# Optimization experiments

Hardware: AMD Instinct MI355X
Metric: run time of the kernel (lower is better)

Reference implementation:

```python
import jax, jax.numpy as jnp
import numpy as np

L, N, D_IN = 4, 2048, 1024
H, DH = 8, 64
INNER = H * DH          # 512
D_OUT = D_IN            # out_dim defaults to input_dim
SCALE = DH ** -0.5


def setup_inputs() -> dict:
    key = jax.random.key(0)
    ks = jax.random.split(key, 7)
    x = jax.random.normal(ks[0], (L, N, D_IN), jnp.float32)
    # torch Linear weights are [out_features, in_features]; xavier-ish scale
    Wq = jax.random.normal(ks[1], (INNER, D_IN), jnp.float32) * 0.03
    Wk = jax.random.normal(ks[2], (INNER, D_IN), jnp.float32) * 0.03
    Wv = jax.random.normal(ks[3], (INNER, D_IN), jnp.float32) * 0.03
    Wo = jax.random.normal(ks[4], (D_OUT, INNER), jnp.float32) * 0.03
    bo = jnp.zeros((D_OUT,), jnp.float32)
    # boolean key-padding mask [L, n]; ensure at least one valid key per row
    mask = jax.random.uniform(ks[5], (L, N)) < 0.9
    mask = mask.at[:, 0].set(True)
    return {"x": x, "Wq": Wq, "Wk": Wk, "Wv": Wv, "Wo": Wo, "bo": bo, "mask": mask}


def reference(x, Wq, Wk, Wv, Wo, bo, mask):
    # projections (Linear: y = x @ W^T), split heads: L n (h d) -> l h n d
    def split_heads(t):
        return t.reshape(L, N, H, DH).transpose(0, 2, 1, 3)

    q = split_heads(jnp.einsum('lnd,ed->lne', x, Wq))
    k = split_heads(jnp.einsum('lnd,ed->lne', x, Wk))  # context defaults to x
    v = split_heads(jnp.einsum('lnd,ed->lne', x, Wv))

    sim = jnp.einsum('lhnd,lhmd->lhnm', q, k) * SCALE   # [L,H,N,N]
    neg = -jnp.finfo(sim.dtype).max
    sim = jnp.where(mask[:, None, None, :], sim, neg)   # mask over key dim
    attn = jax.nn.softmax(sim, axis=-1)

    out = jnp.einsum('lhnm,lhmd->lhnd', attn, v)        # [L,H,N,DH]
    out = out.transpose(0, 2, 1, 3).reshape(L, N, INNER)
    return out @ Wo.T + bo                               # [L,N,D_OUT]
```

## Files before the change

kernel.cpp:

```cpp
#include <hip/hip_runtime.h>
#include <hip/hip_bf16.h>

#define L_DIM 4
#define N_DIM 2048
#define DIN   1024
#define H_DIM 8
#define DH    64
#define INNER 512

typedef __attribute__((ext_vector_type(8))) short short8;
typedef __attribute__((ext_vector_type(4))) float f32x4;

__device__ __forceinline__ unsigned short f2bf(float f) {
  unsigned u = __builtin_bit_cast(unsigned, f);
  u += 0x7fffu + ((u >> 16) & 1u);
  return (unsigned short)(u >> 16);
}

__device__ __forceinline__ unsigned pack2(float a, float b) {
  unsigned ua = __builtin_bit_cast(unsigned, a) + 0x8000u;
  unsigned ub = __builtin_bit_cast(unsigned, b) + 0x8000u;
  return (ua >> 16) | (ub & 0xffff0000u);
}

typedef __attribute__((address_space(3))) unsigned int lds_uint;
typedef const __attribute__((address_space(1))) unsigned int glob_uint;
__device__ __forceinline__ void gl_lds16(const unsigned short* g,
                                         unsigned short* l) {
  __builtin_amdgcn_global_load_lds((glob_uint*)g, (lds_uint*)l, 16, 0, 0);
}

__global__ void cast_all(const float* __restrict__ x,
                         const float* __restrict__ wq,
                         const float* __restrict__ wk,
                         const float* __restrict__ wv,
                         const float* __restrict__ wo,
                         unsigned short* __restrict__ xb,
                         unsigned short* __restrict__ w3,
                         unsigned short* __restrict__ wob,
                         const unsigned char* __restrict__ mraw,
                         float* __restrict__ bias) {
  __shared__ int votes[2];
  int bid = blockIdx.x, t = threadIdx.x;
  if (bid == 10240) {
    if (t < 2) votes[t] = 0;
    __syncthreads();
    const unsigned int* m32 = (const unsigned int*)mraw;
    int anyf = 0, any8 = 0;
    for (int i = t; i < 2048; i += 256) {
      unsigned w = m32[i];
      if (w == 0x3f800000u) anyf = 1;
      if (w & 0xffffff00u) any8 = 1;
    }
    if (anyf) atomicOr(&votes[0], 1);
    if (any8) atomicOr(&votes[1], 1);
    __syncthreads();
    int fmt = votes[0] ? 2 : (votes[1] ? 1 : 0);
    for (int i = t; i < L_DIM * N_DIM; i += 256) {
      int mv;
      if (fmt == 2)      mv = ((const float*)mraw)[i] != 0.0f;
      else if (fmt == 1) mv = mraw[i] != 0;
      else               mv = ((const int*)mraw)[i] != 0;
      bias[i] = mv ? 0.0f : -1e30f;
    }
    return;
  }
  int i = (bid * 256 + t) * 4;
  const float* src; unsigned short* dst; int off;
  if (i < 8388608)      { src = x;  dst = xb;           off = i; }
  else if (i < 8912896) { src = wq; dst = w3;           off = i - 8388608; }
  else if (i < 9437184) { src = wk; dst = w3 + 524288;  off = i - 8912896; }
  else if (i < 9961472) { src = wv; dst = w3 + 1048576; off = i - 9437184; }
  else                  { src = wo; dst = wob;          off = i - 9961472; }
  float4 f = *(const float4*)(src + off);
  ushort4 o4;
  o4.x = f2bf(f.x); o4.y = f2bf(f.y); o4.z = f2bf(f.z); o4.w = f2bf(f.w);
  *(ushort4*)(dst + off) = o4;
}

__launch_bounds__(256, 2)
__global__ void gemm_qkv(const unsigned short* __restrict__ xb,
                         const unsigned short* __restrict__ w3,
                         unsigned short* __restrict__ qp,
                         unsigned short* __restrict__ kp,
                         unsigned short* __restrict__ vtp) {
  __shared__ __align__(16) unsigned short Sh[8704];
  unsigned short* As = Sh;
  unsigned short* Bs = Sh + 4096;
  const int tid = threadIdx.x, lane = tid & 63, wid = tid >> 6;
  const int l16 = lane & 15, quad = lane >> 4;
  const int wm = wid >> 1, wn = wid & 1;
  const int m0 = blockIdx.x * 128, n0 = blockIdx.y * 128;

  f32x4 acc[4][4] = {};
  for (int kt = 0; kt < DIN; kt += 32) {
    __syncthreads();
#pragma unroll
    for (int it = 0; it < 2; ++it) {
      int c = it * 256 + wid * 64 + lane;
      int row = c >> 2, kseg = c & 3;
      unsigned short* lbase = &As[(it * 256 + wid * 64) * 8];
      gl_lds16(&xb[(m0 + row) * DIN + kt + kseg * 8], lbase);
      unsigned short* lbase2 = &Bs[(it * 256 + wid * 64) * 8];
      gl_lds16(&w3[(n0 + row) * DIN + kt + kseg * 8], lbase2);
    }
    __syncthreads();
    short8 af[4], bf[4];
#pragma unroll
    for (int mt = 0; mt < 4; ++mt)
      af[mt] = *(const short8*)&As[(wm * 64 + mt * 16 + l16) * 32 + quad * 8];
#pragma unroll
    for (int nt = 0; nt < 4; ++nt)
      bf[nt] = *(const short8*)&Bs[(wn * 64 + nt * 16 + l16) * 32 + quad * 8];
#pragma unroll
    for (int mt = 0; mt < 4; ++mt)
#pragma unroll
      for (int nt = 0; nt < 4; ++nt)
        acc[mt][nt] = __builtin_amdgcn_mfma_f32_16x16x32_bf16(
            af[mt], bf[nt], acc[mt][nt], 0, 0, 0);
  }
  if (blockIdx.y >= 8) {
    const int l = m0 >> 11, mloc = m0 & 2047;
#pragma unroll
    for (int chunk = 0; chunk < 2; ++chunk) {
      __syncthreads();
      if (wn == chunk) {
#pragma unroll
        for (int mt = 0; mt < 4; ++mt)
#pragma unroll
          for (int nt = 0; nt < 4; ++nt) {
            int col = nt * 16 + l16;
            int rowb = wm * 64 + mt * 16 + quad * 4;
            ushort4 pv;
            pv.x = f2bf(acc[mt][nt][0]);
            pv.y = f2bf(acc[mt][nt][1]);
            pv.z = f2bf(acc[mt][nt][2]);
            pv.w = f2bf(acc[mt][nt][3]);
            *(ushort4*)&Sh[col * 136 + rowb] = pv;
          }
      }
      __syncthreads();
      int hh = ((n0 + chunk * 64) & 511) >> 6;
#pragma unroll
      for (int it = 0; it < 4; ++it) {
        int c = it * 256 + tid;
        int cl = c >> 4, seg = c & 15;
        short8 vv = *(const short8*)&Sh[cl * 136 + seg * 8];
        *(short8*)&vtp[((size_t)((l * H_DIM + hh) * DH + cl)) * N_DIM + mloc +
                       seg * 8] = vv;
      }
    }
  } else {
#pragma unroll
    for (int mt = 0; mt < 4; ++mt)
#pragma unroll
      for (int nt = 0; nt < 4; ++nt)
#pragma unroll
        for (int r = 0; r < 4; ++r) {
          int grow = m0 + wm * 64 + mt * 16 + quad * 4 + r;
          int gcol = n0 + wn * 64 + nt * 16 + l16;
          unsigned short bv = f2bf(acc[mt][nt][r]);
          int h = (gcol & 511) >> 6, d = gcol & 63;
          int l = grow >> 11, n = grow & 2047;
          unsigned short* dst = (gcol >> 9) ? kp : qp;
          dst[(((l * H_DIM + h) * N_DIM + n) * DH) + d] = bv;
        }
  }
}

#define PW_S 128
__launch_bounds__(256, 2)
__global__ void attn_kernel(const unsigned short* __restrict__ qg,
                            const unsigned short* __restrict__ kg,
                            const unsigned short* __restrict__ vtg,
                            const float* __restrict__ bias,
                            unsigned short* __restrict__ aout) {
  __shared__ __align__(16) unsigned short Ks[128 * 64];
  __shared__ __align__(16) unsigned short Vs[64 * 128];
  __shared__ __align__(16) unsigned short Pw[128 * PW_S];
  const int tid = threadIdx.x, lane = tid & 63, wid = tid >> 6;
  const int l16 = lane & 15, quad = lane >> 4;
  const int bid = blockIdx.x;
  const int xcd = bid & 7, j = bid >> 3;
  const int lh = xcd * 4 + (j >> 4);
  const int q0 = (j & 15) << 7;
  const int l = lh >> 3, h = lh & 7;
  const unsigned short* Qb = qg + (size_t)lh * N_DIM * DH;
  const unsigned short* Kb = kg + (size_t)lh * N_DIM * DH;
  const unsigned short* Vt = vtg + (size_t)lh * DH * N_DIM;
  const float* bl = bias + l * N_DIM;

  short8 qf[2][2];
#pragma unroll
  for (int mt = 0; mt < 2; ++mt)
#pragma unroll
    for (int ks = 0; ks < 2; ++ks)
      qf[mt][ks] = *(const short8*)&Qb[(q0 + wid * 32 + mt * 16 + l16) * DH +
                                       ks * 32 + quad * 8];

  f32x4 o[2][4] = {};
  float lsum[2] = {0.f, 0.f};

  for (int kv = 0; kv < N_DIM; kv += 128) {
    __syncthreads();
#pragma unroll
    for (int it = 0; it < 4; ++it) {
      int cb = it * 256 + wid * 64;
      int c = cb + lane;
      int key = c >> 3, sl = c & 7, gs = (sl + key) & 7;
      gl_lds16(&Kb[(kv + key) * DH + gs * 8], &Ks[cb * 8]);
      int d = c >> 4, sv = c & 15, gv = (sv + d) & 15;
      gl_lds16(&Vt[(size_t)d * N_DIM + kv + gv * 8], &Vs[cb * 8]);
    }
    __syncthreads();

    f32x4 sc[2][8] = {};
#pragma unroll
    for (int nt = 0; nt < 8; ++nt)
#pragma unroll
      for (int ks = 0; ks < 2; ++ks) {
        int s = (ks * 4 + quad - l16) & 7;
        short8 kf = *(const short8*)&Ks[(nt * 16 + l16) * 64 + s * 8];
#pragma unroll
        for (int mt = 0; mt < 2; ++mt)
          sc[mt][nt] = __builtin_amdgcn_mfma_f32_16x16x32_bf16(
              kf, qf[mt][ks], sc[mt][nt], 0, 0, 0);
      }
#pragma unroll
    for (int mt = 0; mt < 2; ++mt) {
      unsigned short* pr = &Pw[(wid * 32 + mt * 16 + l16) * PW_S];
#pragma unroll
      for (int nt = 0; nt < 8; ++nt) {
        float4 b4 = *(const float4*)&bl[kv + nt * 16 + quad * 4];
        float p0 = __expf(fmaf(sc[mt][nt][0], 0.125f, b4.x));
        float p1 = __expf(fmaf(sc[mt][nt][1], 0.125f, b4.y));
        float p2 = __expf(fmaf(sc[mt][nt][2], 0.125f, b4.z));
        float p3 = __expf(fmaf(sc[mt][nt][3], 0.125f, b4.w));
        lsum[mt] += (p0 + p1) + (p2 + p3);
        uint2 pk = make_uint2(pack2(p0, p1), pack2(p2, p3));
        int gk = nt * 2 + (quad >> 1);
        int s = (gk + l16) & 15;
        *(uint2*)&pr[s * 8 + (quad & 1) * 4] = pk;
      }
    }
#pragma unroll
    for (int g = 0; g < 4; ++g) {
      short8 pa[2];
#pragma unroll
      for (int mt = 0; mt < 2; ++mt) {
        int sp = (g * 4 + quad + l16) & 15;
        pa[mt] = *(const short8*)&Pw[(wid * 32 + mt * 16 + l16) * PW_S +
                                     sp * 8];
      }
#pragma unroll
      for (int nt = 0; nt < 4; ++nt) {
        int dd = nt * 16 + l16;
        int sv2 = (g * 4 + quad - l16) & 15;
        short8 vb = *(const short8*)&Vs[dd * 128 + sv2 * 8];
#pragma unroll
        for (int mt = 0; mt < 2; ++mt)
          o[mt][nt] = __builtin_amdgcn_mfma_f32_16x16x32_bf16(
              pa[mt], vb, o[mt][nt], 0, 0, 0);
      }
    }
  }
#pragma unroll
  for (int mt = 0; mt < 2; ++mt) {
    lsum[mt] += __shfl_xor(lsum[mt], 16);
    lsum[mt] += __shfl_xor(lsum[mt], 32);
  }
#pragma unroll
  for (int mt = 0; mt < 2; ++mt)
#pragma unroll
    for (int r = 0; r < 4; ++r) {
      float inv = 1.f / __shfl(lsum[mt], quad * 4 + r);
      int row = q0 + wid * 32 + mt * 16 + quad * 4 + r;
#pragma unroll
      for (int nt = 0; nt < 4; ++nt)
        aout[(size_t)(l * N_DIM + row) * INNER + h * DH + nt * 16 + l16] =
            f2bf(o[mt][nt][r] * inv);
    }
}

__launch_bounds__(256, 2)
__global__ void gemm_out(const unsigned short* __restrict__ a,
                         const unsigned short* __restrict__ wo,
                         const float* __restrict__ bo,
                         float* __restrict__ out) {
  __shared__ unsigned short As[128 * 32];
  __shared__ unsigned short Bs[128 * 32];
  const int tid = threadIdx.x, lane = tid & 63, wid = tid >> 6;
  const int l16 = lane & 15, quad = lane >> 4;
  const int wm = wid >> 1, wn = wid & 1;
  const int m0 = blockIdx.x * 128, n0 = blockIdx.y * 128;

  f32x4 acc[4][4] = {};
  for (int kt = 0; kt < INNER; kt += 32) {
    __syncthreads();
#pragma unroll
    for (int it = 0; it < 2; ++it) {
      int c = it * 256 + wid * 64 + lane;
      int row = c >> 2, kseg = c & 3;
      unsigned short* lbase = &As[(it * 256 + wid * 64) * 8];
      gl_lds16(&a[(m0 + row) * INNER + kt + kseg * 8], lbase);
      unsigned short* lbase2 = &Bs[(it * 256 + wid * 64) * 8];
      gl_lds16(&wo[(n0 + row) * INNER + kt + kseg * 8], lbase2);
    }
    __syncthreads();
    short8 af[4], bf[4];
#pragma unroll
    for (int mt = 0; mt < 4; ++mt)
      af[mt] = *(const short8*)&As[(wm * 64 + mt * 16 + l16) * 32 + quad * 8];
#pragma unroll
    for (int nt = 0; nt < 4; ++nt)
      bf[nt] = *(const short8*)&Bs[(wn * 64 + nt * 16 + l16) * 32 + quad * 8];
#pragma unroll
    for (int mt = 0; mt < 4; ++mt)
#pragma unroll
      for (int nt = 0; nt < 4; ++nt)
        acc[mt][nt] = __builtin_amdgcn_mfma_f32_16x16x32_bf16(
            af[mt], bf[nt], acc[mt][nt], 0, 0, 0);
  }
#pragma unroll
  for (int mt = 0; mt < 4; ++mt)
#pragma unroll
    for (int nt = 0; nt < 4; ++nt)
#pragma unroll
      for (int r = 0; r < 4; ++r) {
        int grow = m0 + wm * 64 + mt * 16 + quad * 4 + r;
        int gcol = n0 + wn * 64 + nt * 16 + l16;
        out[(size_t)grow * DIN + gcol] = acc[mt][nt][r] + bo[gcol];
      }
}

extern "C" void kernel_launch(void* const* d_in, const int* in_sizes, int n_in,
                              void* d_out, int out_size, void* d_ws,
                              size_t ws_size, hipStream_t stream) {
  const float* x  = (const float*)d_in[0];
  const float* Wq = (const float*)d_in[1];
  const float* Wk = (const float*)d_in[2];
  const float* Wv = (const float*)d_in[3];
  const float* Wo = (const float*)d_in[4];
  const float* bo = (const float*)d_in[5];
  const unsigned char* mask = (const unsigned char*)d_in[6];
  float* out = (float*)d_out;

  char* ws = (char*)d_ws;
  unsigned short* xb  = (unsigned short*)(ws + 0);
  unsigned short* w3  = (unsigned short*)(ws + 16777216);
  unsigned short* wob = (unsigned short*)(ws + 19922944);
  unsigned short* q   = (unsigned short*)(ws + 20971520);
  unsigned short* k   = (unsigned short*)(ws + 29360128);
  unsigned short* vt  = (unsigned short*)(ws + 37748736);
  unsigned short* att = (unsigned short*)(ws + 46137344);
  float* bias         = (float*)(ws + 54525952);

  cast_all<<<10241, 256, 0, stream>>>(x, Wq, Wk, Wv, Wo, xb, w3, wob, mask,
                                      bias);
  gemm_qkv<<<dim3(64, 12), 256, 0, stream>>>(xb, w3, q, k, vt);
  attn_kernel<<<512, 256, 0, stream>>>(q, k, vt, bias, att);
  gemm_out<<<dim3(64, 8), 256, 0, stream>>>(att, wob, bo, out);
}
```

Measured before the change: 218.5 us.

## Double-buffer K/V tiles in attention and split score tile into halves

The attention kernel now double-buffers the K and V shared-memory tiles, prefetching the next 128-key block while computing on the current one, which drops one barrier per iteration. The score/softmax/PV work is split into two 64-key halves so the probability scratch buffer halves in size and fewer score registers are live. The GEMM kernels' launch bounds are raised to ask for three blocks per SIMD. LDS use in attention grows (two K and two V buffers, about 80KB), which may cut occupancy, and the tighter register budget in the GEMMs risks spills.

Measured after the change: 212.7 us. 2.6% less time.

```diff
diff --git a/kernel.cpp b/kernel.cpp
--- a/kernel.cpp
+++ b/kernel.cpp
@@ -78,7 +78,7 @@
   *(ushort4*)(dst + off) = o4;
 }
 
-__launch_bounds__(256, 2)
+__launch_bounds__(256, 3)
 __global__ void gemm_qkv(const unsigned short* __restrict__ xb,
                          const unsigned short* __restrict__ w3,
                          unsigned short* __restrict__ qp,
@@ -168,15 +168,15 @@
   }
 }
 
-#define PW_S 128
+#define PW_S 64
 __launch_bounds__(256, 2)
 __global__ void attn_kernel(const unsigned short* __restrict__ qg,
                             const unsigned short* __restrict__ kg,
                             const unsigned short* __restrict__ vtg,
                             const float* __restrict__ bias,
                             unsigned short* __restrict__ aout) {
-  __shared__ __align__(16) unsigned short Ks[128 * 64];
-  __shared__ __align__(16) unsigned short Vs[64 * 128];
+  __shared__ __align__(16) unsigned short Ks[2][128 * 64];
+  __shared__ __align__(16) unsigned short Vs[2][64 * 128];
   __shared__ __align__(16) unsigned short Pw[128 * PW_S];
   const int tid = threadIdx.x, lane = tid & 63, wid = tid >> 6;
   const int l16 = lane & 15, quad = lane >> 4;
@@ -201,66 +201,85 @@
   f32x4 o[2][4] = {};
   float lsum[2] = {0.f, 0.f};
 
-  for (int kv = 0; kv < N_DIM; kv += 128) {
-    __syncthreads();
-#pragma unroll
-    for (int it = 0; it < 4; ++it) {
-      int cb = it * 256 + wid * 64;
-      int c = cb + lane;
-      int key = c >> 3, sl = c & 7, gs = (sl + key) & 7;
-      gl_lds16(&Kb[(kv + key) * DH + gs * 8], &Ks[cb * 8]);
-      int d = c >> 4, sv = c & 15, gv = (sv + d) & 15;
-      gl_lds16(&Vt[(size_t)d * N_DIM + kv + gv * 8], &Vs[cb * 8]);
-    }
-    __syncthreads();
-
-    f32x4 sc[2][8] = {};
-#pragma unroll
-    for (int nt = 0; nt < 8; ++nt)
-#pragma unroll
-      for (int ks = 0; ks < 2; ++ks) {
-        int s = (ks * 4 + quad - l16) & 7;
-        short8 kf = *(const short8*)&Ks[(nt * 16 + l16) * 64 + s * 8];
-#pragma unroll
-        for (int mt = 0; mt < 2; ++mt)
-          sc[mt][nt] = __builtin_amdgcn_mfma_f32_16x16x32_bf16(
-              kf, qf[mt][ks], sc[mt][nt], 0, 0, 0);
-      }
-#pragma unroll
-    for (int mt = 0; mt < 2; ++mt) {
-      unsigned short* pr = &Pw[(wid * 32 + mt * 16 + l16) * PW_S];
-#pragma unroll
-      for (int nt = 0; nt < 8; ++nt) {
-        float4 b4 = *(const float4*)&bl[kv + nt * 16 + quad * 4];
-        float p0 = __expf(fmaf(sc[mt][nt][0], 0.125f, b4.x));
-        float p1 = __expf(fmaf(sc[mt][nt][1], 0.125f, b4.y));
-        float p2 = __expf(fmaf(sc[mt][nt][2], 0.125f, b4.z));
-        float p3 = __expf(fmaf(sc[mt][nt][3], 0.125f, b4.w));
-        lsum[mt] += (p0 + p1) + (p2 + p3);
-        uint2 pk = make_uint2(pack2(p0, p1), pack2(p2, p3));
-        int gk = nt * 2 + (quad >> 1);
-        int s = (gk + l16) & 15;
-        *(uint2*)&pr[s * 8 + (quad & 1) * 4] = pk;
-      }
-    }
-#pragma unroll
-    for (int g = 0; g < 4; ++g) {
-      short8 pa[2];
+#pragma unroll
+  for (int it = 0; it < 4; ++it) {
+    int cb = it * 256 + wid * 64;
+    int c = cb + lane;
+    int key = c >> 3, sl = c & 7, gs = (sl + key) & 7;
+    gl_lds16(&Kb[key * DH + gs * 8], &Ks[0][cb * 8]);
+    int d = c >> 4, sv = c & 15, gv = (sv + d) & 15;
+    gl_lds16(&Vt[(size_t)d * N_DIM + gv * 8], &Vs[0][cb * 8]);
+  }
+
+  for (int t = 0; t < 16; ++t) {
+    const int kv = t << 7, buf = t & 1;
+    __syncthreads();
+    if (t < 15) {
+      int kv2 = kv + 128, b2 = buf ^ 1;
+#pragma unroll
+      for (int it = 0; it < 4; ++it) {
+        int cb = it * 256 + wid * 64;
+        int c = cb + lane;
+        int key = c >> 3, sl = c & 7, gs = (sl + key) & 7;
+        gl_lds16(&Kb[(kv2 + key) * DH + gs * 8], &Ks[b2][cb * 8]);
+        int d = c >> 4, sv = c & 15, gv = (sv + d) & 15;
+        gl_lds16(&Vt[(size_t)d * N_DIM + kv2 + gv * 8], &Vs[b2][cb * 8]);
+      }
+    }
+    const unsigned short* Kst = Ks[buf];
+    const unsigned short* Vst = Vs[buf];
+
+#pragma unroll
+    for (int hf = 0; hf < 2; ++hf) {
+      f32x4 sc[2][4] = {};
+#pragma unroll
+      for (int nt = 0; nt < 4; ++nt)
+#pragma unroll
+        for (int ks = 0; ks < 2; ++ks) {
+          int s = (ks * 4 + quad - l16) & 7;
+          short8 kf = *(const short8*)&Kst[(hf * 64 + nt * 16 + l16) * 64 +
+                                           s * 8];
+#pragma unroll
+          for (int mt = 0; mt < 2; ++mt)
+            sc[mt][nt] = __builtin_amdgcn_mfma_f32_16x16x32_bf16(
+                kf, qf[mt][ks], sc[mt][nt], 0, 0, 0);
+        }
 #pragma unroll
       for (int mt = 0; mt < 2; ++mt) {
-        int sp = (g * 4 + quad + l16) & 15;
-        pa[mt] = *(const short8*)&Pw[(wid * 32 + mt * 16 + l16) * PW_S +
-                                     sp * 8];
-      }
-#pragma unroll
-      for (int nt = 0; nt < 4; ++nt) {
-        int dd = nt * 16 + l16;
-        int sv2 = (g * 4 + quad - l16) & 15;
-        short8 vb = *(const short8*)&Vs[dd * 128 + sv2 * 8];
-#pragma unroll
-        for (int mt = 0; mt < 2; ++mt)
-          o[mt][nt] = __builtin_amdgcn_mfma_f32_16x16x32_bf16(
-              pa[mt], vb, o[mt][nt], 0, 0, 0);
+        unsigned short* pr = &Pw[(wid * 32 + mt * 16 + l16) * PW_S];
+#pragma unroll
+        for (int nt = 0; nt < 4; ++nt) {
+          float4 b4 = *(const float4*)&bl[kv + hf * 64 + nt * 16 + quad * 4];
+          float p0 = __expf(fmaf(sc[mt][nt][0], 0.125f, b4.x));
+          float p1 = __expf(fmaf(sc[mt][nt][1], 0.125f, b4.y));
+          float p2 = __expf(fmaf(sc[mt][nt][2], 0.125f, b4.z));
+          float p3 = __expf(fmaf(sc[mt][nt][3], 0.125f, b4.w));
+          lsum[mt] += (p0 + p1) + (p2 + p3);
+          uint2 pk = make_uint2(pack2(p0, p1), pack2(p2, p3));
+          int gk = nt * 2 + (quad >> 1);
+          int s = (gk + l16) & 7;
+          *(uint2*)&pr[s * 8 + (quad & 1) * 4] = pk;
+        }
+      }
+#pragma unroll
+      for (int g = 0; g < 2; ++g) {
+        short8 pa[2];
+#pragma unroll
+        for (int mt = 0; mt < 2; ++mt) {
+          int sp = (g * 4 + quad + l16) & 7;
+          pa[mt] = *(const short8*)&Pw[(wid * 32 + mt * 16 + l16) * PW_S +
+                                       sp * 8];
+        }
+#pragma unroll
+        for (int nt = 0; nt < 4; ++nt) {
+          int dd = nt * 16 + l16;
+          int sv2 = (hf * 8 + g * 4 + quad - l16) & 15;
+          short8 vb = *(const short8*)&Vst[dd * 128 + sv2 * 8];
+#pragma unroll
+          for (int mt = 0; mt < 2; ++mt)
+            o[mt][nt] = __builtin_amdgcn_mfma_f32_16x16x32_bf16(
+                pa[mt], vb, o[mt][nt], 0, 0, 0);
+        }
       }
     }
   }
@@ -282,7 +301,7 @@
     }
 }
 
-__launch_bounds__(256, 2)
+__launch_bounds__(256, 3)
 __global__ void gemm_out(const unsigned short* __restrict__ a,
                          const unsigned short* __restrict__ wo,
                          const float* __restrict__ bo,
```
